# Optimization experiments

Measured on AMD Instinct MI355X. Metric: run time of the kernel, lower is better.

## Reference

```python
import jax, jax.numpy as jnp
import numpy as np

EMBED_DIM = 1024
NUM_HEADS = 16
HEAD_DIM = EMBED_DIM // NUM_HEADS


def setup_inputs() -> dict:
    key = jax.random.key(0)
    ks = jax.random.split(key, 5)
    B, T, C = 2, 2048, EMBED_DIM
    s_in = 1.0 / np.sqrt(C)
    x = jax.random.normal(ks[0], (B, T, C), dtype=jnp.float32)
    W_qkv = jax.random.normal(ks[1], (C, 3 * C), dtype=jnp.float32) * s_in
    b_qkv = jnp.zeros((3 * C,), dtype=jnp.float32)
    W_out = jax.random.normal(ks[2], (C, C), dtype=jnp.float32) * s_in
    b_out = jnp.zeros((C,), dtype=jnp.float32)
    return {"x": x, "W_qkv": W_qkv, "b_qkv": b_qkv, "W_out": W_out, "b_out": b_out}


def reference(x, W_qkv, b_qkv, W_out, b_out):
    B, T, C = x.shape
    H, D = NUM_HEADS, HEAD_DIM
    qkv = x @ W_qkv + b_qkv                      # [B,T,3C]
    qkv = qkv.reshape(B, T, 3, H, D)
    q = jnp.transpose(qkv[:, :, 0], (0, 2, 1, 3))  # [B,H,T,D]
    k = jnp.transpose(qkv[:, :, 1], (0, 2, 1, 3))
    v = jnp.transpose(qkv[:, :, 2], (0, 2, 1, 3))
    scores = jnp.einsum('bhtd,bhsd->bhts', q, k) / np.sqrt(D).astype(jnp.float32)
    attn = jax.nn.softmax(scores, axis=-1)
    ctx = jnp.einsum('bhts,bhsd->bhtd', attn, v)   # [B,H,T,D]
    ctx = jnp.transpose(ctx, (0, 2, 1, 3)).reshape(B, T, C)
    return ctx @ W_out + b_out
```

## Files before the change

kernel.cpp:

```cpp
#include <hip/hip_runtime.h>
#include <hip/hip_bf16.h>


typedef __attribute__((ext_vector_type(8)))  short short8;
typedef __attribute__((ext_vector_type(4)))  float floatx4;
typedef __attribute__((ext_vector_type(16))) float floatx16;

__device__ inline ushort f2bf(float f) {
    union { __hip_bfloat16 h; ushort u; } c; c.h = __float2bfloat16(f); return c.u;
}

__device__ inline uint cvt_pk_bf16(float a, float b) {
    uint r;
    asm("v_cvt_pk_bf16_f32 %0, %1, %2" : "=v"(r) : "v"(a), "v"(b));
    return r;
}

__device__ inline void gld16(const ushort* g, ushort* l) {
    __builtin_amdgcn_global_load_lds(
        (__attribute__((address_space(1))) void*)(g),
        (__attribute__((address_space(3))) void*)(l), 16, 0, 0);
}

__device__ inline void tile_transpose(const float* __restrict__ src, ushort* __restrict__ dst,
                                      int R, int C, int rt, int ct, int t, ushort* L)
{
    const int row = t >> 2, cc = (t & 3) * 16;
    const float* sp = src + (long)(rt * 64 + row) * C + ct * 64 + cc;
    ushort tmp[16];
    #pragma unroll
    for (int i = 0; i < 4; i++) {
        float4 v = *(const float4*)(sp + i * 4);
        tmp[i*4+0]=f2bf(v.x); tmp[i*4+1]=f2bf(v.y); tmp[i*4+2]=f2bf(v.z); tmp[i*4+3]=f2bf(v.w);
    }
    *(uint4*)&L[row * 72 + cc]     = *(uint4*)&tmp[0];
    *(uint4*)&L[row * 72 + cc + 8] = *(uint4*)&tmp[8];
    __syncthreads();
    const int c = t >> 2, rc = (t & 3) * 16;
    ushort o[16];
    #pragma unroll
    for (int j = 0; j < 16; j++) o[j] = L[(rc + j) * 72 + c];
    ushort* dp = dst + (long)(ct * 64 + c) * R + rt * 64 + rc;
    *(uint4*)dp       = *(uint4*)&o[0];
    *(uint4*)(dp + 8) = *(uint4*)&o[8];
}

__global__ __launch_bounds__(256) void prep_kernel(
    const float* __restrict__ x, const float* __restrict__ Wqkv, const float* __restrict__ Wout,
    ushort* __restrict__ xb, ushort* __restrict__ wqkvT, ushort* __restrict__ woutT)
{
    __shared__ __align__(16) ushort L[64 * 72];
    const int bid = blockIdx.x, t = threadIdx.x;
    if (bid < 2048) {
        long i = ((long)bid * 256 + t) * 8;
        float4 a = *(const float4*)(x + i);
        float4 b = *(const float4*)(x + i + 4);
        ushort tmp[8] = { f2bf(a.x), f2bf(a.y), f2bf(a.z), f2bf(a.w),
                          f2bf(b.x), f2bf(b.y), f2bf(b.z), f2bf(b.w) };
        *(uint4*)(xb + i) = *(uint4*)tmp;
    } else if (bid < 2048 + 768) {
        int idx = bid - 2048;
        tile_transpose(Wqkv, wqkvT, 1024, 3072, idx & 15, idx >> 4, t, L);
    } else {
        int idx = bid - 2048 - 768;
        tile_transpose(Wout, woutT, 1024, 1024, idx & 15, idx >> 4, t, L);
    }
}

#define QSCALE 0.18033688011112042f

__global__ __launch_bounds__(256, 3) void qkv_gemm_kernel(
    const ushort* __restrict__ A, const ushort* __restrict__ Bt,
    const float* __restrict__ bias,
    ushort* __restrict__ qbuf, ushort* __restrict__ kbuf, ushort* __restrict__ vtG)
{
    __shared__ __align__(16) ushort SMEM[16384];

    const int t = threadIdx.x;
    const int w = t >> 6, lane = t & 63;
    const int r = lane & 15, qq = lane >> 4;
    const int wm = w >> 1, wn = w & 1;

    const int id = blockIdx.x;
    const int xcd = id & 7, cidx = id >> 3;
    const int lx = cidx % 12, ly = cidx / 12;
    const int bx = (xcd & 1) * 12 + lx;
    const int by = (xcd >> 1) * 8 + ly;
    const int rowBase = by * 128, colBase = bx * 128;

    const int s_row = lane >> 2, s_k = (lane & 3) * 8;
    const ushort* aS = A  + (long)(rowBase + w * 32 + s_row) * 1024 + s_k;
    const ushort* bS = Bt + (long)(colBase + w * 32 + s_row) * 1024 + s_k;

    floatx4 acc[4][4] = {};

    gld16(aS,             SMEM + w * 1024);
    gld16(aS + 16 * 1024, SMEM + w * 1024 + 512);
    gld16(bS,             SMEM + 4096 + w * 1024);
    gld16(bS + 16 * 1024, SMEM + 4096 + w * 1024 + 512);
    __syncthreads();

    #pragma unroll 2
    for (int k = 0; k < 32; k++) {
        ushort* cur = SMEM + (k & 1) * 8192;
        if (k < 31) {
            ushort* nxt = SMEM + ((k + 1) & 1) * 8192;
            const int ko = (k + 1) * 32;
            gld16(aS + ko,             nxt + w * 1024);
            gld16(aS + ko + 16 * 1024, nxt + w * 1024 + 512);
            gld16(bS + ko,             nxt + 4096 + w * 1024);
            gld16(bS + ko + 16 * 1024, nxt + 4096 + w * 1024 + 512);
        }
        short8 af[4], bf4[4];
        #pragma unroll
        for (int tm = 0; tm < 4; tm++) af[tm]  = *(const short8*)&cur[(wm * 64 + tm * 16 + r) * 32 + qq * 8];
        #pragma unroll
        for (int tn = 0; tn < 4; tn++) bf4[tn] = *(const short8*)&cur[4096 + (wn * 64 + tn * 16 + r) * 32 + qq * 8];
        #pragma unroll
        for (int tm = 0; tm < 4; tm++)
            #pragma unroll
            for (int tn = 0; tn < 4; tn++)
                acc[tm][tn] = __builtin_amdgcn_mfma_f32_16x16x32_bf16(af[tm], bf4[tn], acc[tm][tn], 0, 0, 0);
        __syncthreads();
    }

    if (colBase < 2048) {
        #pragma unroll
        for (int tn = 0; tn < 4; tn++) {
            int col = colBase + wn * 64 + tn * 16 + r;
            float bvv = bias[col];
            #pragma unroll
            for (int tm = 0; tm < 4; tm++) {
                #pragma unroll
                for (int reg = 0; reg < 4; reg++) {
                    int row = rowBase + wm * 64 + tm * 16 + qq * 4 + reg;
                    float val = acc[tm][tn][reg] + bvv;
                    if (colBase < 1024) qbuf[(long)row * 1024 + col]        = f2bf(val * QSCALE);
                    else                kbuf[(long)row * 1024 + col - 1024] = f2bf(val);
                }
            }
        }
    } else {
        ushort* L = SMEM;
        #pragma unroll
        for (int hh = 0; hh < 2; hh++) {
            __syncthreads();
            if (wn == hh) {
                #pragma unroll
                for (int tn = 0; tn < 4; tn++) {
                    int vc = tn * 16 + r;
                    float bvv = bias[colBase + wn * 64 + vc];
                    #pragma unroll
                    for (int tm = 0; tm < 4; tm++) {
                        int row0 = wm * 64 + tm * 16 + qq * 4;
                        ushort q4[4] = { f2bf(acc[tm][tn][0] + bvv), f2bf(acc[tm][tn][1] + bvv),
                                         f2bf(acc[tm][tn][2] + bvv), f2bf(acc[tm][tn][3] + bvv) };
                        *(uint2*)&L[vc * 136 + row0] = *(uint2*)q4;
                    }
                }
            }
            __syncthreads();
            int d = t >> 2, tq = (t & 3) * 32;
            int h_loc = ((colBase - 2048) >> 6) + hh;
            long vtrow = (long)((rowBase >> 11) * 16 + h_loc) * 64 + d;
            ushort* dst = vtG + vtrow * 2048 + (rowBase & 2047) + tq;
            #pragma unroll
            for (int i = 0; i < 4; i++)
                *(uint4*)(dst + 8 * i) = *(uint4*)&L[d * 136 + tq + 8 * i];
        }
    }
}

__global__ __launch_bounds__(256) void out_gemm_kernel(
    const ushort* __restrict__ A, const ushort* __restrict__ Bt,
    const float* __restrict__ bias, float* __restrict__ out)
{
    __shared__ __align__(16) ushort SMEM[12288];

    const int t = threadIdx.x;
    const int w = t >> 6, lane = t & 63;
    const int r = lane & 15, qq = lane >> 4;
    const int wm = w >> 1, wn = w & 1;

    const int id = blockIdx.x;
    const int xcd = id & 7, cidx = id >> 3;
    const int bx = (xcd & 1) * 8 + (cidx & 7);
    const int by = (xcd >> 1) * 8 + (cidx >> 3);
    const int rowBase = by * 128, colBase = bx * 64;

    const int s_row = lane >> 2, s_k = (lane & 3) * 8;
    const ushort* aS = A  + (long)(rowBase + w * 32 + s_row) * 1024 + s_k;
    const ushort* bS = Bt + (long)(colBase + w * 16 + s_row) * 1024 + s_k;

    floatx4 acc[4][2] = {};

    gld16(aS,             SMEM + w * 1024);
    gld16(aS + 16 * 1024, SMEM + w * 1024 + 512);
    gld16(bS,             SMEM + 4096 + w * 512);
    __syncthreads();

    #pragma unroll 2
    for (int k = 0; k < 32; k++) {
        ushort* cur = SMEM + (k & 1) * 6144;
        if (k < 31) {
            ushort* nxt = SMEM + ((k + 1) & 1) * 6144;
            const int ko = (k + 1) * 32;
            gld16(aS + ko,             nxt + w * 1024);
            gld16(aS + ko + 16 * 1024, nxt + w * 1024 + 512);
            gld16(bS + ko,             nxt + 4096 + w * 512);
        }
        short8 af[4], bf2[2];
        #pragma unroll
        for (int tm = 0; tm < 4; tm++) af[tm]  = *(const short8*)&cur[(wm * 64 + tm * 16 + r) * 32 + qq * 8];
        #pragma unroll
        for (int tn = 0; tn < 2; tn++) bf2[tn] = *(const short8*)&cur[4096 + (wn * 32 + tn * 16 + r) * 32 + qq * 8];
        #pragma unroll
        for (int tm = 0; tm < 4; tm++)
            #pragma unroll
            for (int tn = 0; tn < 2; tn++)
                acc[tm][tn] = __builtin_amdgcn_mfma_f32_16x16x32_bf16(af[tm], bf2[tn], acc[tm][tn], 0, 0, 0);
        __syncthreads();
    }

    #pragma unroll
    for (int tn = 0; tn < 2; tn++) {
        int col = colBase + wn * 32 + tn * 16 + r;
        float bvv = bias[col];
        #pragma unroll
        for (int tm = 0; tm < 4; tm++) {
            #pragma unroll
            for (int reg = 0; reg < 4; reg++) {
                int row = rowBase + wm * 64 + tm * 16 + qq * 4 + reg;
                out[(long)row * 1024 + col] = acc[tm][tn][reg] + bvv;
            }
        }
    }
}

__global__ __launch_bounds__(512, 2) void attn_kernel(
    ushort* __restrict__ qbuf, const ushort* __restrict__ kbuf,
    const ushort* __restrict__ vt)
{
    __shared__ __align__(16) ushort SM[2][2][64 * 72];

    const int t = threadIdx.x;
    const int w = t >> 6, lane = t & 63;
    const int m32 = lane & 31, hi = lane >> 5;

    const int id = blockIdx.x;
    const int j = id >> 3;
    const int bh = (id & 7) * 4 + (j >> 3);
    const int qt = j & 7;
    const int b = bh >> 4, h = bh & 15;
    const long qrow = (long)(b * 2048 + qt * 256 + w * 32 + m32);

    short8 qfrag[4];
    #pragma unroll
    for (int dc = 0; dc < 4; dc++)
        qfrag[dc] = *(const short8*)(qbuf + qrow * 1024 + h * 64 + dc * 16 + hi * 8);

    short8 vones;
    #pragma unroll
    for (int i = 0; i < 8; i++) vones[i] = (short)0x3F80;

    const int srow = t >> 3, scol = (t & 7) * 8;
    const ushort* kP = kbuf + (long)(b * 2048 + srow) * 1024 + h * 64 + scol;
    const ushort* vP = vt + (long)(bh * 64 + srow) * 2048 + scol;

    floatx16 o[2] = {};
    floatx16 lacc = {};

    uint4 kr0, vr0;

    kr0 = *(const uint4*)kP;
    vr0 = *(const uint4*)vP;
    *(uint4*)&SM[0][0][srow * 72 + scol] = kr0;
    *(uint4*)&SM[0][1][srow * 72 + scol] = vr0;
    kr0 = *(const uint4*)(kP + 64 * 1024);
    vr0 = *(const uint4*)(vP + 64);
    __syncthreads();

    #pragma unroll 2
    for (int tt = 0; tt < 32; tt++) {
        ushort* Ks = SM[tt & 1][0];
        ushort* Vs = SM[tt & 1][1];

        floatx16 s[2] = {};
        __builtin_amdgcn_s_setprio(1);
        #pragma unroll
        for (int c = 0; c < 2; c++) {
            #pragma unroll
            for (int dc = 0; dc < 4; dc++) {
                short8 kf = *(const short8*)&Ks[(c * 32 + m32) * 72 + dc * 16 + hi * 8];
                s[c] = __builtin_amdgcn_mfma_f32_32x32x16_bf16(kf, qfrag[dc], s[c], 0, 0, 0);
            }
        }
        __builtin_amdgcn_s_setprio(0);

        if (tt < 31) {
            *(uint4*)&SM[(tt + 1) & 1][0][srow * 72 + scol] = kr0;
            *(uint4*)&SM[(tt + 1) & 1][1][srow * 72 + scol] = vr0;
            if (tt < 30) {
                kr0 = *(const uint4*)(kP + (long)(tt + 2) * 64 * 1024);
                vr0 = *(const uint4*)(vP + (tt + 2) * 64);
            }
        }

        uint pk[2][8];
        #pragma unroll
        for (int c = 0; c < 2; c++) {
            #pragma unroll
            for (int i = 0; i < 8; i++) {
                float p0 = __builtin_amdgcn_exp2f(s[c][2 * i]);
                float p1 = __builtin_amdgcn_exp2f(s[c][2 * i + 1]);
                pk[c][i] = cvt_pk_bf16(p0, p1);
            }
        }

        __builtin_amdgcn_s_setprio(1);
        #pragma unroll
        for (int c = 0; c < 2; c++) {
            #pragma unroll
            for (int kc = 0; kc < 2; kc++) {
                uint a0 = pk[c][4 * kc + 0], b0 = pk[c][4 * kc + 2];
                asm("v_permlane32_swap_b32 %0, %1" : "+v"(a0), "+v"(b0));
                uint a1 = pk[c][4 * kc + 1], b1 = pk[c][4 * kc + 3];
                asm("v_permlane32_swap_b32 %0, %1" : "+v"(a1), "+v"(b1));
                union { uint u[4]; short8 s8; } cv;
                cv.u[0] = a0; cv.u[1] = a1; cv.u[2] = b0; cv.u[3] = b1;
                #pragma unroll
                for (int dt = 0; dt < 2; dt++) {
                    short8 vf = *(const short8*)&Vs[(dt * 32 + m32) * 72 + c * 32 + kc * 16 + hi * 8];
                    o[dt] = __builtin_amdgcn_mfma_f32_32x32x16_bf16(vf, cv.s8, o[dt], 0, 0, 0);
                }
                lacc = __builtin_amdgcn_mfma_f32_32x32x16_bf16(vones, cv.s8, lacc, 0, 0, 0);
            }
        }
        __builtin_amdgcn_s_setprio(0);

        __syncthreads();
    }

    float inv = 1.f / lacc[0];

    #pragma unroll
    for (int dt = 0; dt < 2; dt++) {
        #pragma unroll
        for (int g = 0; g < 4; g++) {
            ushort tmp[4] = { f2bf(o[dt][4*g+0] * inv), f2bf(o[dt][4*g+1] * inv),
                              f2bf(o[dt][4*g+2] * inv), f2bf(o[dt][4*g+3] * inv) };
            *(uint2*)(qbuf + qrow * 1024 + h * 64 + dt * 32 + g * 8 + hi * 4) = *(uint2*)tmp;
        }
    }
}

extern "C" void kernel_launch(void* const* d_in, const int* in_sizes, int n_in,
                              void* d_out, int out_size, void* d_ws, size_t ws_size,
                              hipStream_t stream) {
    const float* x     = (const float*)d_in[0];
    const float* W_qkv = (const float*)d_in[1];
    const float* b_qkv = (const float*)d_in[2];
    const float* W_out = (const float*)d_in[3];
    const float* b_out = (const float*)d_in[4];
    float* out = (float*)d_out;

    ushort* qbuf  = (ushort*)d_ws;
    ushort* kbuf  = qbuf + (size_t)4096 * 1024;
    ushort* vt    = kbuf + (size_t)4096 * 1024;
    ushort* woutT = vt + (size_t)2048 * 2048;
    ushort* wqkvT = woutT + (size_t)1024 * 1024;

    ushort* xb    = (ushort*)d_out;

    dim3 blk(256);
    prep_kernel<<<3072, blk, 0, stream>>>(x, W_qkv, W_out, xb, wqkvT, woutT);
    qkv_gemm_kernel<<<768, blk, 0, stream>>>(xb, wqkvT, b_qkv, qbuf, kbuf, vt);
    attn_kernel<<<256, dim3(512), 0, stream>>>(qbuf, kbuf, vt);
    out_gemm_kernel<<<512, blk, 0, stream>>>(qbuf, woutT, b_out, out);
}
```

Before: 178.9 us.

## Quad-buffer K/V tiles in LDS and synchronize every second iteration

The attention kernel's LDS staging grows from two to four K/V buffers. Two tiles are now prefetched into registers and stored in pairs, so the block barrier runs only on odd iterations, halving the number of __syncthreads. The aim is to cut barrier stalls and hide global-load latency behind more work. In exchange it uses twice the LDS per block and more VGPRs for the extra prefetch registers, which could hurt occupancy at two blocks per CU.

```diff
diff --git a/kernel.cpp b/kernel.cpp
--- a/kernel.cpp
+++ b/kernel.cpp
@@ -241,7 +241,7 @@
     ushort* __restrict__ qbuf, const ushort* __restrict__ kbuf,
     const ushort* __restrict__ vt)
 {
-    __shared__ __align__(16) ushort SM[2][2][64 * 72];
+    __shared__ __align__(16) ushort SM[4][2][64 * 72];
 
     const int t = threadIdx.x;
     const int w = t >> 6, lane = t & 63;
@@ -270,20 +270,22 @@
     floatx16 o[2] = {};
     floatx16 lacc = {};
 
-    uint4 kr0, vr0;
-
-    kr0 = *(const uint4*)kP;
-    vr0 = *(const uint4*)vP;
-    *(uint4*)&SM[0][0][srow * 72 + scol] = kr0;
-    *(uint4*)&SM[0][1][srow * 72 + scol] = vr0;
-    kr0 = *(const uint4*)(kP + 64 * 1024);
-    vr0 = *(const uint4*)(vP + 64);
+    uint4 krA, vrA, krB, vrB;
+
+    krA = *(const uint4*)kP;                vrA = *(const uint4*)vP;
+    *(uint4*)&SM[0][0][srow * 72 + scol] = krA;
+    *(uint4*)&SM[0][1][srow * 72 + scol] = vrA;
+    krB = *(const uint4*)(kP + 64 * 1024);  vrB = *(const uint4*)(vP + 64);
+    *(uint4*)&SM[1][0][srow * 72 + scol] = krB;
+    *(uint4*)&SM[1][1][srow * 72 + scol] = vrB;
+    krA = *(const uint4*)(kP + 2L * 64 * 1024); vrA = *(const uint4*)(vP + 2 * 64);
+    krB = *(const uint4*)(kP + 3L * 64 * 1024); vrB = *(const uint4*)(vP + 3 * 64);
     __syncthreads();
 
-    #pragma unroll 2
+    #pragma unroll 4
     for (int tt = 0; tt < 32; tt++) {
-        ushort* Ks = SM[tt & 1][0];
-        ushort* Vs = SM[tt & 1][1];
+        ushort* Ks = SM[tt & 3][0];
+        ushort* Vs = SM[tt & 3][1];
 
         floatx16 s[2] = {};
         __builtin_amdgcn_s_setprio(1);
@@ -297,12 +299,16 @@
         }
         __builtin_amdgcn_s_setprio(0);
 
-        if (tt < 31) {
-            *(uint4*)&SM[(tt + 1) & 1][0][srow * 72 + scol] = kr0;
-            *(uint4*)&SM[(tt + 1) & 1][1][srow * 72 + scol] = vr0;
-            if (tt < 30) {
-                kr0 = *(const uint4*)(kP + (long)(tt + 2) * 64 * 1024);
-                vr0 = *(const uint4*)(vP + (tt + 2) * 64);
+        if ((tt & 1) == 0 && tt < 30) {
+            *(uint4*)&SM[(tt + 2) & 3][0][srow * 72 + scol] = krA;
+            *(uint4*)&SM[(tt + 2) & 3][1][srow * 72 + scol] = vrA;
+            *(uint4*)&SM[(tt + 3) & 3][0][srow * 72 + scol] = krB;
+            *(uint4*)&SM[(tt + 3) & 3][1][srow * 72 + scol] = vrB;
+            if (tt < 28) {
+                krA = *(const uint4*)(kP + (long)(tt + 4) * 64 * 1024);
+                vrA = *(const uint4*)(vP + (tt + 4) * 64);
+                krB = *(const uint4*)(kP + (long)(tt + 5) * 64 * 1024);
+                vrB = *(const uint4*)(vP + (tt + 5) * 64);
             }
         }
 
@@ -338,7 +344,7 @@
         }
         __builtin_amdgcn_s_setprio(0);
 
-        __syncthreads();
+        if (tt & 1) __syncthreads();
     }
 
     float inv = 1.f / lacc[0];
```

Result: slower. 185.1 us (+3.5%).
